# Kernel optimization log

Hardware: AMD Instinct MI355X
Metric: run time of the kernel (lower is better)

Reference implementation:

```python
import jax, jax.numpy as jnp
import numpy as np


def setup_inputs() -> dict:
    key = jax.random.key(0)
    k1, k2, k3 = jax.random.split(key, 3)
    B, F, E = 512, 64, 32
    feature = jax.random.normal(k1, (B, F, E), dtype=jnp.float32)
    # params initialized ~ N(0, 0.01) as in the torch module
    weight = 0.01 * jax.random.normal(k2, (F, E, E), dtype=jnp.float32)
    weightLeft = 0.01 * jax.random.normal(k3, (F, F), dtype=jnp.float32)
    return {"feature": feature, "weight": weight, "weightLeft": weightLeft}


def reference(feature, weight, weightLeft):
    # biLinear[b,f,d] = sum_e feature[b,f,e] * weight[f,e,d]   (per-feature ExE matmul)
    biLinear = jnp.einsum('bfe,fed->bfd', feature, weight)  # [B,F,E]
    # interaction[b,f,g,e] = biLinear[b,f,e] * feature[b,g,e] * weightLeft[f,g]
    out = (biLinear[:, :, None, :] * feature[:, None, :, :]) * weightLeft[None, :, :, None]
    return out  # [B,F,F,E]
```

## Files before the change

kernel.cpp:

```cpp
#include <hip/hip_runtime.h>


#define BDIM 512
#define FDIM 64
#define EDIM 32

__global__ __launch_bounds__(256) void bilinear_v2_kernel(
    const float* __restrict__ feature,
    const float* __restrict__ weight,
    const float* __restrict__ weightLeft,
    float* __restrict__ out)
{
    const int bf = blockIdx.x;
    const int f  = bf & (FDIM - 1);
    const int b  = bf >> 6;

    __shared__ float bl[EDIM];
    __shared__ float wl[FDIM];

    const int t = threadIdx.x;

    if (t < EDIM) {
        const float* fp = feature + (size_t)bf * EDIM;
        const float* wp = weight + (size_t)f * EDIM * EDIM;
        float acc = 0.f;
        #pragma unroll
        for (int e = 0; e < EDIM; ++e) {
            acc += fp[e] * wp[e * EDIM + t];
        }
        bl[t] = acc;
    } else if (t >= 64 && t < 64 + FDIM) {
        wl[t - 64] = weightLeft[f * FDIM + (t - 64)];
    }
    __syncthreads();

    float*       op = out     + (size_t)bf * (FDIM * EDIM);
    const float* fb = feature + (size_t)b  * (FDIM * EDIM);

    #pragma unroll
    for (int i = 0; i < 2; ++i) {
        const int idx4 = t + i * 256;
        const int e4   = idx4 & (EDIM / 4 - 1);
        const int g    = idx4 >> 3;

        const float4 fv  = reinterpret_cast<const float4*>(fb)[idx4];
        const float4 blv = reinterpret_cast<const float4*>(bl)[e4];
        const float  w   = wl[g];

        float4 o;
        o.x = blv.x * fv.x * w;
        o.y = blv.y * fv.y * w;
        o.z = blv.z * fv.z * w;
        o.w = blv.w * fv.w * w;
        reinterpret_cast<float4*>(op)[idx4] = o;
    }
}

extern "C" void kernel_launch(void* const* d_in, const int* in_sizes, int n_in,
                              void* d_out, int out_size, void* d_ws, size_t ws_size,
                              hipStream_t stream) {
    const float* feature    = (const float*)d_in[0];
    const float* weight     = (const float*)d_in[1];
    const float* weightLeft = (const float*)d_in[2];
    float* out = (float*)d_out;

    const int nblocks = BDIM * FDIM;
    bilinear_v2_kernel<<<nblocks, 256, 0, stream>>>(feature, weight, weightLeft, out);
}
```

Before: 271.4 us.

## Process eight features per block with shared-memory staging of feature row

Each block now handles 8 f-values for one batch instead of one, staging the batch's full feature tile and eight weightLeft rows in shared memory. All 256 threads compute the bilinear products (8x32) instead of only 32, and each thread writes 16 float4s. This cuts the block count eightfold and removes the repeated global reads of the feature tile, at the cost of more shared memory and fewer, longer-running blocks.

```diff
diff --git a/kernel.cpp b/kernel.cpp
--- a/kernel.cpp
+++ b/kernel.cpp
@@ -4,6 +4,8 @@
 #define BDIM 512
 #define FDIM 64
 #define EDIM 32
+#define FPB  8
+#define NFG  (FDIM / FPB)
 
 __global__ __launch_bounds__(256) void bilinear_v2_kernel(
     const float* __restrict__ feature,
@@ -11,41 +13,57 @@
     const float* __restrict__ weightLeft,
     float* __restrict__ out)
 {
-    const int bf = blockIdx.x;
-    const int f  = bf & (FDIM - 1);
-    const int b  = bf >> 6;
+    const int blk = blockIdx.x;
+    const int fg  = blk & (NFG - 1);
+    const int b   = blk >> 3;
+    const int f0  = fg * FPB;
+    const int t   = threadIdx.x;
 
-    __shared__ float bl[EDIM];
-    __shared__ float wl[FDIM];
+    __shared__ float s_feat[FDIM * EDIM];
+    __shared__ float s_bl[FPB * EDIM];
+    __shared__ float s_wl[FPB * FDIM];
 
-    const int t = threadIdx.x;
+    const float* fb = feature + (size_t)b * (FDIM * EDIM);
 
-    if (t < EDIM) {
-        const float* fp = feature + (size_t)bf * EDIM;
-        const float* wp = weight + (size_t)f * EDIM * EDIM;
+    #pragma unroll
+    for (int i = 0; i < 2; ++i) {
+        const int idx = t + i * 256;
+        reinterpret_cast<float4*>(s_feat)[idx] =
+            reinterpret_cast<const float4*>(fb)[idx];
+    }
+
+    #pragma unroll
+    for (int i = 0; i < 2; ++i) {
+        const int idx = t + i * 256;
+        s_wl[idx] = weightLeft[(f0 + (idx >> 6)) * FDIM + (idx & 63)];
+    }
+
+    {
+        const int fl = t >> 5;
+        const int d  = t & 31;
+        const int f  = f0 + fl;
+        const float* fp = fb + f * EDIM;
+        const float* wp = weight + (size_t)f * EDIM * EDIM + d;
         float acc = 0.f;
         #pragma unroll
-        for (int e = 0; e < EDIM; ++e) {
-            acc += fp[e] * wp[e * EDIM + t];
-        }
-        bl[t] = acc;
-    } else if (t >= 64 && t < 64 + FDIM) {
-        wl[t - 64] = weightLeft[f * FDIM + (t - 64)];
+        for (int e = 0; e < EDIM; ++e)
+            acc += fp[e] * wp[e * EDIM];
+        s_bl[fl * EDIM + d] = acc;
     }
     __syncthreads();
 
-    float*       op = out     + (size_t)bf * (FDIM * EDIM);
-    const float* fb = feature + (size_t)b  * (FDIM * EDIM);
+    float* op = out + ((size_t)b * FDIM + f0) * (FDIM * EDIM);
 
     #pragma unroll
-    for (int i = 0; i < 2; ++i) {
+    for (int i = 0; i < 16; ++i) {
         const int idx4 = t + i * 256;
-        const int e4   = idx4 & (EDIM / 4 - 1);
-        const int g    = idx4 >> 3;
+        const int e4   = idx4 & 7;
+        const int g    = (idx4 >> 3) & 63;
+        const int fl   = idx4 >> 9;
 
-        const float4 fv  = reinterpret_cast<const float4*>(fb)[idx4];
-        const float4 blv = reinterpret_cast<const float4*>(bl)[e4];
-        const float  w   = wl[g];
+        const float4 fv  = reinterpret_cast<const float4*>(s_feat)[g * 8 + e4];
+        const float4 blv = reinterpret_cast<const float4*>(s_bl)[fl * 8 + e4];
+        const float  w   = s_wl[fl * 64 + g];
 
         float4 o;
         o.x = blv.x * fv.x * w;
@@ -64,6 +82,6 @@
     const float* weightLeft = (const float*)d_in[2];
     float* out = (float*)d_out;
 
-    const int nblocks = BDIM * FDIM;
+    const int nblocks = BDIM * NFG;
     bilinear_v2_kernel<<<nblocks, 256, 0, stream>>>(feature, weight, weightLeft, out);
 }
```

After: 268.8 us. About the same (-0.9%).
